# Optimization experiments

Measured on AMD Instinct MI355X. Metric: run time of the kernel, lower is better.

## Reference

```python
import jax, jax.numpy as jnp
import numpy as np


def _rel_agg(h, src, dst, n_nodes):
    """GraphConv(norm='right', weight=False): sum messages at dst, divide by in-degree."""
    msg = jax.ops.segment_sum(h[src], dst, num_segments=n_nodes)          # [N, D]
    deg = jax.ops.segment_sum(jnp.ones(src.shape, h.dtype), dst, num_segments=n_nodes)
    return msg / jnp.maximum(deg, 1.0)[:, None]


def setup_inputs() -> dict:
    key = jax.random.key(0)
    ks = jax.random.split(key, 6)
    N, R, E, D, C = 50000, 4, 400000, 256, 64
    embed = jax.random.normal(ks[0], (N, D), jnp.float32)
    src = jax.random.randint(ks[1], (R, E), 0, N, dtype=jnp.int32)
    dst = jax.random.randint(ks[2], (R, E), 0, N, dtype=jnp.int32)
    b0 = jnp.zeros((D,), jnp.float32)
    w1 = jax.random.normal(ks[3], (R, D, D), jnp.float32) * (1.0 / np.sqrt(D))
    b1 = jnp.zeros((D,), jnp.float32)
    w_out = jax.random.normal(ks[4], (R, D, C), jnp.float32) * (1.0 / np.sqrt(D))
    b_out = jnp.zeros((C,), jnp.float32)
    return {"embed": embed, "src": src, "dst": dst, "b0": b0,
            "w1": w1, "b1": b1, "w_out": w_out, "b_out": b_out}


def reference(embed, src, dst, b0, w1, b1, w_out, b_out):
    N = embed.shape[0]
    R = src.shape[0]
    # Layer 0: weight=False -> sum of per-relation right-normalized aggregations, bias, relu
    h = jnp.zeros_like(embed)
    for r in range(R):
        h = h + _rel_agg(embed, src[r], dst[r], N)
    h = jax.nn.relu(h + b0)
    # Hidden layer: aggregate then per-relation dense weight, summed over relations
    h2 = jnp.zeros((N, w1.shape[2]), embed.dtype)
    for r in range(R):
        h2 = h2 + _rel_agg(h, src[r], dst[r], N) @ w1[r]
    h2 = jax.nn.relu(h2 + b1)
    # Output layer: same, no activation
    out = jnp.zeros((N, w_out.shape[2]), embed.dtype)
    for r in range(R):
        out = out + _rel_agg(h2, src[r], dst[r], N) @ w_out[r]
    return out + b_out
```

## Files before the change

### kernel.cpp

```cpp
#include <hip/hip_runtime.h>


typedef unsigned short ushort_t;
using f32x4  = __attribute__((ext_vector_type(4))) float;
using short8 = __attribute__((ext_vector_type(8))) short;

__device__ inline float bf2f(unsigned s) { return __uint_as_float(s << 16); }
__device__ inline unsigned short f2bf(float f) {
  unsigned u = __float_as_uint(f);
  u += 0x7FFF + ((u >> 16) & 1);
  return (unsigned short)(u >> 16);
}
__device__ inline void u4tof8(const uint4 v, float f[8]) {
  f[0] = bf2f(v.x & 0xffffu); f[1] = bf2f(v.x >> 16);
  f[2] = bf2f(v.y & 0xffffu); f[3] = bf2f(v.y >> 16);
  f[4] = bf2f(v.z & 0xffffu); f[5] = bf2f(v.z >> 16);
  f[6] = bf2f(v.w & 0xffffu); f[7] = bf2f(v.w >> 16);
}

__global__ void rank_k(const int* __restrict__ dst, int E, int Nn,
                       int* __restrict__ cnt, int* __restrict__ rank) {
  int base = (blockIdx.x * blockDim.x + threadIdx.x) * 8;
  int r = blockIdx.y;
  if (base >= E) return;
  const int* dr = dst + (size_t)r * E;
  int* cr = cnt + (size_t)r * Nn;
  int* rk = rank + (size_t)r * E;
  if (base + 7 < E) {
    const int4 a = *reinterpret_cast<const int4*>(dr + base);
    const int4 b = *reinterpret_cast<const int4*>(dr + base + 4);
    int4 ra, rb;
    ra.x = atomicAdd(&cr[a.x], 1); ra.y = atomicAdd(&cr[a.y], 1);
    ra.z = atomicAdd(&cr[a.z], 1); ra.w = atomicAdd(&cr[a.w], 1);
    rb.x = atomicAdd(&cr[b.x], 1); rb.y = atomicAdd(&cr[b.y], 1);
    rb.z = atomicAdd(&cr[b.z], 1); rb.w = atomicAdd(&cr[b.w], 1);
    *reinterpret_cast<int4*>(rk + base) = ra;
    *reinterpret_cast<int4*>(rk + base + 4) = rb;
  } else {
    for (int j = 0; j < 8 && base + j < E; j++)
      rk[base + j] = atomicAdd(&cr[dr[base + j]], 1);
  }
}

__global__ __launch_bounds__(1024) void scanA_k(const int* __restrict__ degcnt, int M,
                                                int* __restrict__ rowptr,
                                                int* __restrict__ blocksum) {
  __shared__ int sm[1024];
  int t = threadIdx.x;
  int g = blockIdx.x * 1024 + t;
  int v = (g < M) ? degcnt[g] : 0;
  sm[t] = v;
  __syncthreads();
  for (int off = 1; off < 1024; off <<= 1) {
    int u = (t >= off) ? sm[t - off] : 0;
    __syncthreads();
    sm[t] += u;
    __syncthreads();
  }
  if (g < M) rowptr[g] = sm[t] - v;
  if (t == 1023) blocksum[blockIdx.x] = sm[1023];
}

__global__ __launch_bounds__(1024) void scanB_k(int* __restrict__ blocksum, int nb) {
  __shared__ int sm[1024];
  int t = threadIdx.x;
  int v = (t < nb) ? blocksum[t] : 0;
  sm[t] = v;
  __syncthreads();
  for (int off = 1; off < 1024; off <<= 1) {
    int u = (t >= off) ? sm[t - off] : 0;
    __syncthreads();
    sm[t] += u;
    __syncthreads();
  }
  if (t < nb) blocksum[t] = sm[t] - v;
}

__global__ __launch_bounds__(1024) void scanC_k(const int* __restrict__ degcnt, int M,
                                                const int* __restrict__ blocksum,
                                                int* __restrict__ rowptr,
                                                float* __restrict__ invdeg) {
  int g = blockIdx.x * 1024 + threadIdx.x;
  if (g < M) {
    int val = rowptr[g] + blocksum[blockIdx.x];
    int dd = degcnt[g];
    rowptr[g] = val;
    invdeg[g] = 1.0f / (float)(dd > 0 ? dd : 1);
    if (g == M - 1) rowptr[M] = val + dd;
  }
}

__global__ void fill_k(const int* __restrict__ src, const int* __restrict__ dst,
                       const int* __restrict__ rank,
                       const int* __restrict__ rowptr, int E, int Nn,
                       int* __restrict__ eidx) {
  int base = (blockIdx.x * blockDim.x + threadIdx.x) * 8;
  int r = blockIdx.y;
  if (base >= E) return;
  const int* dr = dst + (size_t)r * E;
  const int* sr = src + (size_t)r * E;
  const int* rk = rank + (size_t)r * E;
  const int* rp = rowptr + (size_t)r * Nn;
  if (base + 7 < E) {
    const int4 d0 = *reinterpret_cast<const int4*>(dr + base);
    const int4 d1 = *reinterpret_cast<const int4*>(dr + base + 4);
    const int4 s0 = *reinterpret_cast<const int4*>(sr + base);
    const int4 s1 = *reinterpret_cast<const int4*>(sr + base + 4);
    const int4 k0 = *reinterpret_cast<const int4*>(rk + base);
    const int4 k1 = *reinterpret_cast<const int4*>(rk + base + 4);
    eidx[rp[d0.x] + k0.x] = s0.x;
    eidx[rp[d0.y] + k0.y] = s0.y;
    eidx[rp[d0.z] + k0.z] = s0.z;
    eidx[rp[d0.w] + k0.w] = s0.w;
    eidx[rp[d1.x] + k1.x] = s1.x;
    eidx[rp[d1.y] + k1.y] = s1.y;
    eidx[rp[d1.z] + k1.z] = s1.z;
    eidx[rp[d1.w] + k1.w] = s1.w;
  } else {
    for (int j = 0; j < 8 && base + j < E; j++)
      eidx[rp[dr[base + j]] + rk[base + j]] = sr[base + j];
  }
}

__global__ void f2bf_vec_k(const float* __restrict__ in, ushort_t* __restrict__ out,
                           long n4) {
  long i = (long)blockIdx.x * blockDim.x + threadIdx.x;
  if (i < n4) {
    float4 v = *reinterpret_cast<const float4*>(in + i * 4);
    ushort4 o; o.x = f2bf(v.x); o.y = f2bf(v.y); o.z = f2bf(v.z); o.w = f2bf(v.w);
    *reinterpret_cast<ushort4*>(out + i * 4) = o;
  }
}

__global__ void wtrans_k(const float* __restrict__ w, ushort_t* __restrict__ wt,
                         int K, int Nd, int total) {
  int tid = blockIdx.x * blockDim.x + threadIdx.x;
  if (tid < total) {
    int k = tid % K;
    int j = tid / K;
    int c = j % Nd;
    int r = j / Nd;
    wt[(size_t)j * K + k] = f2bf(w[((size_t)r * K + k) * Nd + c]);
  }
}

__global__ __launch_bounds__(256) void pull_gather256_k(
    const ushort_t* __restrict__ x, int xpitch, int rsub,
    const int* __restrict__ eidx,
    const int* __restrict__ rowptr, const float* __restrict__ invdeg,
    int R, int Nn, ushort_t* __restrict__ out, const float* __restrict__ bias) {
  int wv = (blockIdx.x * blockDim.x + threadIdx.x) >> 6;
  int lane = threadIdx.x & 63;
  int node = (wv << 1) + (lane >> 5);
  if (node >= Nn) return;
  int col8 = (lane & 31) << 3;
  float s[8] = {};
  for (int r = 0; r < R; r++) {
    const int* rp = rowptr + (size_t)r * Nn;
    int sb = rp[node], e = rp[node + 1];
    size_t rb = (size_t)(r * rsub + col8);
    float p[8] = {};
    for (int i = sb; i < e; i += 4) {
      int i1 = i + 1 < e ? i + 1 : i;
      int i2 = i + 2 < e ? i + 2 : i;
      int i3 = i + 3 < e ? i + 3 : i;
      float m1 = i + 1 < e ? 1.f : 0.f;
      float m2 = i + 2 < e ? 1.f : 0.f;
      float m3 = i + 3 < e ? 1.f : 0.f;
      const uint4 v0 = *reinterpret_cast<const uint4*>(x + (size_t)eidx[i]  * xpitch + rb);
      const uint4 v1 = *reinterpret_cast<const uint4*>(x + (size_t)eidx[i1] * xpitch + rb);
      const uint4 v2 = *reinterpret_cast<const uint4*>(x + (size_t)eidx[i2] * xpitch + rb);
      const uint4 v3 = *reinterpret_cast<const uint4*>(x + (size_t)eidx[i3] * xpitch + rb);
      float a0[8], a1[8], a2[8], a3[8];
      u4tof8(v0, a0); u4tof8(v1, a1); u4tof8(v2, a2); u4tof8(v3, a3);
#pragma unroll
      for (int j = 0; j < 8; j++)
        p[j] += (a0[j] + m1 * a1[j]) + (m2 * a2[j] + m3 * a3[j]);
    }
    float w = invdeg[(size_t)r * Nn + node];
#pragma unroll
    for (int j = 0; j < 8; j++) s[j] += p[j] * w;
  }
  const float4 ba = *reinterpret_cast<const float4*>(bias + col8);
  const float4 bb = *reinterpret_cast<const float4*>(bias + col8 + 4);
  s[0] += ba.x; s[1] += ba.y; s[2] += ba.z; s[3] += ba.w;
  s[4] += bb.x; s[5] += bb.y; s[6] += bb.z; s[7] += bb.w;
  short8 ov;
#pragma unroll
  for (int j = 0; j < 8; j++) ov[j] = (short)f2bf(fmaxf(s[j], 0.f));
  *reinterpret_cast<short8*>(out + ((size_t)node << 8) + col8) = ov;
}

__global__ __launch_bounds__(256) void pull_out64_k(
    const ushort_t* __restrict__ q, int qpitch,
    const int* __restrict__ eidx,
    const int* __restrict__ rowptr, const float* __restrict__ invdeg,
    int R, int Nn, float* __restrict__ out, const float* __restrict__ bias) {
  int node = (blockIdx.x * blockDim.x + threadIdx.x) >> 6;
  if (node >= Nn) return;
  int lane = threadIdx.x & 63;
  int es = lane >> 4;
  int c4 = (lane & 15) << 2;
  float s[4] = {};
  for (int r = 0; r < R; r++) {
    const int* rp = rowptr + (size_t)r * Nn;
    int sb = rp[node], e = rp[node + 1];
    size_t rb = (size_t)((r << 6) + c4);
    float p[4] = {};
    for (int i = sb + es; i < e; i += 4) {
      const uint2 v = *reinterpret_cast<const uint2*>(q + (size_t)eidx[i] * qpitch + rb);
      p[0] += bf2f(v.x & 0xffffu); p[1] += bf2f(v.x >> 16);
      p[2] += bf2f(v.y & 0xffffu); p[3] += bf2f(v.y >> 16);
    }
    float w = invdeg[(size_t)r * Nn + node];
#pragma unroll
    for (int j = 0; j < 4; j++) s[j] += p[j] * w;
  }
#pragma unroll
  for (int j = 0; j < 4; j++) {
    s[j] += __shfl_xor(s[j], 16, 64);
    s[j] += __shfl_xor(s[j], 32, 64);
  }
  if (es == 0) {
    const float4 bv = *reinterpret_cast<const float4*>(bias + c4);
    float4 o;
    o.x = s[0] + bv.x; o.y = s[1] + bv.y; o.z = s[2] + bv.z; o.w = s[3] + bv.w;
    *reinterpret_cast<float4*>(out + ((size_t)node << 6) + c4) = o;
  }
}

template <int FN>
__global__ __launch_bounds__(256) void gemm_mfma_k(
    const ushort_t* __restrict__ A, const ushort_t* __restrict__ Bt,
    ushort_t* __restrict__ Cp, int M, int K, int Nd) {
  __shared__ ushort_t Atile[128][72];
  const int tid = threadIdx.x;
  const int lane = tid & 63;
  const int wid = tid >> 6;
  const int wr = wid >> 1;
  const int wc = wid & 1;
  const int rowBase = blockIdx.y * 128;
  const int colBase = blockIdx.x * (FN * 32);
  const int l15 = lane & 15;
  const int g = lane >> 4;

  f32x4 acc[4][FN] = {};

  const int srow = tid >> 3;
  const int schunk = tid & 7;

  for (int k0 = 0; k0 < K; k0 += 64) {
#pragma unroll
    for (int i = 0; i < 4; i++) {
      int row = srow + i * 32;
      int grow = rowBase + row;
      if (grow >= M) grow = M - 1;
      short8 v = *reinterpret_cast<const short8*>(A + (size_t)grow * K + k0 + schunk * 8);
      *reinterpret_cast<short8*>(&Atile[row][schunk * 8]) = v;
    }
    __syncthreads();
#pragma unroll
    for (int kk = 0; kk < 2; kk++) {
      short8 a[4], b[FN];
#pragma unroll
      for (int m = 0; m < 4; m++)
        a[m] = *reinterpret_cast<const short8*>(&Atile[wr * 64 + m * 16 + l15][kk * 32 + g * 8]);
#pragma unroll
      for (int n = 0; n < FN; n++) {
        int col = colBase + wc * (FN * 16) + n * 16 + l15;
        b[n] = *reinterpret_cast<const short8*>(Bt + (size_t)col * K + k0 + kk * 32 + g * 8);
      }
#pragma unroll
      for (int m = 0; m < 4; m++)
#pragma unroll
        for (int n = 0; n < FN; n++)
          acc[m][n] = __builtin_amdgcn_mfma_f32_16x16x32_bf16(a[m], b[n], acc[m][n], 0, 0, 0);
    }
    __syncthreads();
  }

#pragma unroll
  for (int n = 0; n < FN; n++) {
    int col = colBase + wc * (FN * 16) + n * 16 + l15;
#pragma unroll
    for (int m = 0; m < 4; m++) {
      int row0 = rowBase + wr * 64 + m * 16 + g * 4;
#pragma unroll
      for (int j = 0; j < 4; j++) {
        int row = row0 + j;
        if (row < M) Cp[(size_t)row * Nd + col] = f2bf(acc[m][n][j]);
      }
    }
  }
}

extern "C" void kernel_launch(void* const* d_in, const int* in_sizes, int n_in,
                              void* d_out, int out_size, void* d_ws, size_t ws_size,
                              hipStream_t stream) {
  const float* embed = (const float*)d_in[0];
  const int* src     = (const int*)d_in[1];
  const int* dst     = (const int*)d_in[2];
  const float* b0    = (const float*)d_in[3];
  const float* w1    = (const float*)d_in[4];
  const float* b1    = (const float*)d_in[5];
  const float* w_out = (const float*)d_in[6];
  const float* b_out = (const float*)d_in[7];
  float* out = (float*)d_out;

  const int D = in_sizes[3];
  const int C = in_sizes[7];
  const int N = in_sizes[0] / D;
  const int R = in_sizes[4] / (D * D);
  const int E = in_sizes[1] / R;
  const int M = R * N;
  const int N1 = R * D;
  const int N2 = R * C;

  char* w = (char*)d_ws;
  size_t off = 0;
  auto carve = [&](size_t bytes) -> void* {
    void* p = w + off;
    off += (bytes + 255) & ~(size_t)255;
    return p;
  };
  ushort_t* ebf  = (ushort_t*)carve((size_t)N * D * 2);
  ushort_t* h    = (ushort_t*)carve((size_t)N * D * 2);
  ushort_t* t    = (ushort_t*)carve((size_t)N * N1 * 2);
  ushort_t* w1t  = (ushort_t*)carve((size_t)N1 * D * 2);
  ushort_t* wot  = (ushort_t*)carve((size_t)N2 * D * 2);
  float* invdeg  = (float*)carve((size_t)M * 4);
  int* rowptr    = (int*)carve(((size_t)M + 1) * 4);
  int* degcnt    = (int*)carve((size_t)M * 4);
  int* eidx      = (int*)carve((size_t)R * E * 4);
  int* blocksum  = (int*)carve(1024 * 4);
  ushort_t* h2 = ebf;
  ushort_t* q  = t;
  int* rank = (int*)t;
  (void)n_in; (void)out_size; (void)ws_size;

  hipMemsetAsync(degcnt, 0, (size_t)M * 4, stream);
  dim3 egrid((E + 2047) / 2048, R);
  rank_k<<<egrid, 256, 0, stream>>>(dst, E, N, degcnt, rank);
  int nblkScan = (M + 1023) / 1024;
  scanA_k<<<nblkScan, 1024, 0, stream>>>(degcnt, M, rowptr, blocksum);
  scanB_k<<<1, 1024, 0, stream>>>(blocksum, nblkScan);
  scanC_k<<<nblkScan, 1024, 0, stream>>>(degcnt, M, blocksum, rowptr, invdeg);
  fill_k<<<egrid, 256, 0, stream>>>(src, dst, rank, rowptr, E, N, eidx);

  long n4 = (long)N * D / 4;
  f2bf_vec_k<<<(int)((n4 + 255) / 256), 256, 0, stream>>>(embed, ebf, n4);
  wtrans_k<<<(N1 * D + 255) / 256, 256, 0, stream>>>(w1, w1t, D, D, N1 * D);
  wtrans_k<<<(N2 * D + 255) / 256, 256, 0, stream>>>(w_out, wot, D, C, N2 * D);

  const int pullBlocks2 = ((N + 1) / 2 * 64 + 255) / 256;
  const int pullBlocks1 = (N * 64 + 255) / 256;

  pull_gather256_k<<<pullBlocks2, 256, 0, stream>>>(ebf, D, 0, eidx, rowptr, invdeg,
                                                    R, N, h, b0);

  {
    dim3 grid(N1 / 128, (N + 127) / 128);
    gemm_mfma_k<4><<<grid, 256, 0, stream>>>(h, w1t, t, N, D, N1);
  }
  pull_gather256_k<<<pullBlocks2, 256, 0, stream>>>(t, N1, D, eidx, rowptr, invdeg,
                                                    R, N, h2, b1);

  {
    dim3 grid(N2 / 128, (N + 127) / 128);
    gemm_mfma_k<4><<<grid, 256, 0, stream>>>(h2, wot, q, N, D, N2);
  }
  pull_out64_k<<<pullBlocks1, 256, 0, stream>>>(q, N2, eidx, rowptr, invdeg,
                                                R, N, out, b_out);
}
```

Before: 519.8 us.

## Fuse hidden-layer aggregation and per-relation GEMM into one kernel

The hidden layer now aggregates the 256-wide features first, per relation, into shared memory. It then multiplies them by that relation's weight slice with MFMA and accumulates across relations inside a new kernel. This replaces the separate GEMM that wrote an N x R*D intermediate and the gather that read it back. The aim is to remove that large intermediate round trip and to gather 256-wide rows instead of 1024-wide ones. In exchange the kernel pairs a latency-bound gather phase with a compute phase and separates them with block barriers, and the weight transpose layout changes to match.

After: 571.0 us. 9.8% more time.

```diff
diff --git a/kernel.cpp b/kernel.cpp
--- a/kernel.cpp
+++ b/kernel.cpp
@@ -191,6 +191,97 @@
   *reinterpret_cast<short8*>(out + ((size_t)node << 8) + col8) = ov;
 }
 
+__global__ __launch_bounds__(256) void fused_l1_k(
+    const ushort_t* __restrict__ h,
+    const ushort_t* __restrict__ Bt,
+    const int* __restrict__ eidx,
+    const int* __restrict__ rowptr,
+    const float* __restrict__ invdeg,
+    int R, int Nn,
+    ushort_t* __restrict__ h2,
+    const float* __restrict__ bias) {
+  __shared__ ushort_t hagg[64][264];
+  const int tid = threadIdx.x;
+  const int lane = tid & 63;
+  const int wid = tid >> 6;
+  const int rowBase = blockIdx.x * 64;
+  const int l15 = lane & 15;
+  const int g = lane >> 4;
+  const int col8 = (lane & 31) << 3;
+  const int half = lane >> 5;
+
+  f32x4 acc[4][4] = {};
+
+  for (int r = 0; r < R; r++) {
+    const int* rp = rowptr + (size_t)r * Nn;
+#pragma unroll
+    for (int step = 0; step < 8; step++) {
+      int rowLocal = wid * 16 + step * 2 + half;
+      int node = rowBase + rowLocal;
+      int cn = node < Nn ? node : Nn - 1;
+      int sb = rp[cn], e = rp[cn + 1];
+      float p[8] = {};
+      for (int i = sb; i < e; i += 4) {
+        int i1 = i + 1 < e ? i + 1 : i;
+        int i2 = i + 2 < e ? i + 2 : i;
+        int i3 = i + 3 < e ? i + 3 : i;
+        float m1 = i + 1 < e ? 1.f : 0.f;
+        float m2 = i + 2 < e ? 1.f : 0.f;
+        float m3 = i + 3 < e ? 1.f : 0.f;
+        const uint4 v0 = *reinterpret_cast<const uint4*>(h + ((size_t)eidx[i]  << 8) + col8);
+        const uint4 v1 = *reinterpret_cast<const uint4*>(h + ((size_t)eidx[i1] << 8) + col8);
+        const uint4 v2 = *reinterpret_cast<const uint4*>(h + ((size_t)eidx[i2] << 8) + col8);
+        const uint4 v3 = *reinterpret_cast<const uint4*>(h + ((size_t)eidx[i3] << 8) + col8);
+        float a0[8], a1[8], a2[8], a3[8];
+        u4tof8(v0, a0); u4tof8(v1, a1); u4tof8(v2, a2); u4tof8(v3, a3);
+#pragma unroll
+        for (int j = 0; j < 8; j++)
+          p[j] += (a0[j] + m1 * a1[j]) + (m2 * a2[j] + m3 * a3[j]);
+      }
+      float w = invdeg[(size_t)r * Nn + cn];
+      short8 ov;
+#pragma unroll
+      for (int j = 0; j < 8; j++) ov[j] = (short)f2bf(p[j] * w);
+      *reinterpret_cast<short8*>(&hagg[rowLocal][col8]) = ov;
+    }
+    __syncthreads();
+#pragma unroll
+    for (int ks = 0; ks < 8; ks++) {
+      short8 a[4], b[4];
+#pragma unroll
+      for (int m = 0; m < 4; m++)
+        a[m] = *reinterpret_cast<const short8*>(&hagg[m * 16 + l15][ks * 32 + g * 8]);
+#pragma unroll
+      for (int n = 0; n < 4; n++) {
+        int col = wid * 64 + n * 16 + l15;
+        b[n] = *reinterpret_cast<const short8*>(Bt + ((size_t)col << 10) + (r << 8) + ks * 32 + g * 8);
+      }
+#pragma unroll
+      for (int m = 0; m < 4; m++)
+#pragma unroll
+        for (int n = 0; n < 4; n++)
+          acc[m][n] = __builtin_amdgcn_mfma_f32_16x16x32_bf16(a[m], b[n], acc[m][n], 0, 0, 0);
+    }
+    __syncthreads();
+  }
+
+#pragma unroll
+  for (int n = 0; n < 4; n++) {
+    int col = wid * 64 + n * 16 + l15;
+    float bv = bias[col];
+#pragma unroll
+    for (int m = 0; m < 4; m++) {
+      int row0 = rowBase + m * 16 + g * 4;
+#pragma unroll
+      for (int j = 0; j < 4; j++) {
+        int row = row0 + j;
+        if (row < Nn)
+          h2[((size_t)row << 8) + col] = f2bf(fmaxf(acc[m][n][j] + bv, 0.f));
+      }
+    }
+  }
+}
+
 __global__ __launch_bounds__(256) void pull_out64_k(
     const ushort_t* __restrict__ q, int qpitch,
     const int* __restrict__ eidx,
@@ -268,7 +359,7 @@
 #pragma unroll
       for (int n = 0; n < FN; n++) {
         int col = colBase + wc * (FN * 16) + n * 16 + l15;
-        b[n] = *reinterpret_cast<const short8*>(Bt + (size_t)col * K + k0 + kk * 32 + g * 8);
+        b[n] = *reinterpret_cast<const short8*>(Bt + (size_t)col * K + kk * 32 + k0 + g * 8);
       }
 #pragma unroll
       for (int m = 0; m < 4; m++)
@@ -326,7 +417,7 @@
   ushort_t* ebf  = (ushort_t*)carve((size_t)N * D * 2);
   ushort_t* h    = (ushort_t*)carve((size_t)N * D * 2);
   ushort_t* t    = (ushort_t*)carve((size_t)N * N1 * 2);
-  ushort_t* w1t  = (ushort_t*)carve((size_t)N1 * D * 2);
+  ushort_t* w1t  = (ushort_t*)carve((size_t)D * N1 * 2);
   ushort_t* wot  = (ushort_t*)carve((size_t)N2 * D * 2);
   float* invdeg  = (float*)carve((size_t)M * 4);
   int* rowptr    = (int*)carve(((size_t)M + 1) * 4);
@@ -349,7 +440,7 @@
 
   long n4 = (long)N * D / 4;
   f2bf_vec_k<<<(int)((n4 + 255) / 256), 256, 0, stream>>>(embed, ebf, n4);
-  wtrans_k<<<(N1 * D + 255) / 256, 256, 0, stream>>>(w1, w1t, D, D, N1 * D);
+  wtrans_k<<<(N1 * D + 255) / 256, 256, 0, stream>>>(w1, w1t, N1, D, N1 * D);
   wtrans_k<<<(N2 * D + 255) / 256, 256, 0, stream>>>(w_out, wot, D, C, N2 * D);
 
   const int pullBlocks2 = ((N + 1) / 2 * 64 + 255) / 256;
@@ -358,12 +449,8 @@
   pull_gather256_k<<<pullBlocks2, 256, 0, stream>>>(ebf, D, 0, eidx, rowptr, invdeg,
                                                     R, N, h, b0);
 
-  {
-    dim3 grid(N1 / 128, (N + 127) / 128);
-    gemm_mfma_k<4><<<grid, 256, 0, stream>>>(h, w1t, t, N, D, N1);
-  }
-  pull_gather256_k<<<pullBlocks2, 256, 0, stream>>>(t, N1, D, eidx, rowptr, invdeg,
-                                                    R, N, h2, b1);
+  fused_l1_k<<<(N + 63) / 64, 256, 0, stream>>>(h, w1t, eidx, rowptr, invdeg,
+                                                R, N, h2, b1);
 
   {
     dim3 grid(N2 / 128, (N + 127) / 128);
```

## Build CSR with destination-sliced counting and cursor-based atomic fill

Applied to the files above, without the earlier changes.

Replaces the rank-recording counting pass with a count-only pass, and the rank-based fill with a fill that claims slots through per-node cursor atomics. Both passes split the grid into 8 destination-range slices so each block's atomics hit a narrower node range, which should improve L2 locality on the counter and cursor arrays. The rank buffer and its write and read traffic go away. In exchange, each edge's dst and src are read 8 times, and neighbour order inside each row is no longer deterministic. That may change floating-point summation order in the gather.

Measured after the change: 588.6 us. 1.13x slower.

```diff
diff --git a/kernel.cpp b/kernel.cpp
--- a/kernel.cpp
+++ b/kernel.cpp
@@ -18,27 +18,33 @@
   f[6] = bf2f(v.w & 0xffffu); f[7] = bf2f(v.w >> 16);
 }
 
-__global__ void rank_k(const int* __restrict__ dst, int E, int Nn,
-                       int* __restrict__ cnt, int* __restrict__ rank) {
-  int base = (blockIdx.x * blockDim.x + threadIdx.x) * 8;
+#define EPT 16
+
+__global__ void count_k(const int* __restrict__ dst, int E, int Nn, int nsl,
+                        int* __restrict__ cnt) {
+  int slice = blockIdx.x & 7;
+  int chunk = blockIdx.x >> 3;
   int r = blockIdx.y;
-  if (base >= E) return;
+  int lo = slice * nsl;
+  int hi = lo + nsl; if (hi > Nn) hi = Nn;
   const int* dr = dst + (size_t)r * E;
   int* cr = cnt + (size_t)r * Nn;
-  int* rk = rank + (size_t)r * E;
-  if (base + 7 < E) {
-    const int4 a = *reinterpret_cast<const int4*>(dr + base);
-    const int4 b = *reinterpret_cast<const int4*>(dr + base + 4);
-    int4 ra, rb;
-    ra.x = atomicAdd(&cr[a.x], 1); ra.y = atomicAdd(&cr[a.y], 1);
-    ra.z = atomicAdd(&cr[a.z], 1); ra.w = atomicAdd(&cr[a.w], 1);
-    rb.x = atomicAdd(&cr[b.x], 1); rb.y = atomicAdd(&cr[b.y], 1);
-    rb.z = atomicAdd(&cr[b.z], 1); rb.w = atomicAdd(&cr[b.w], 1);
-    *reinterpret_cast<int4*>(rk + base) = ra;
-    *reinterpret_cast<int4*>(rk + base + 4) = rb;
-  } else {
-    for (int j = 0; j < 8 && base + j < E; j++)
-      rk[base + j] = atomicAdd(&cr[dr[base + j]], 1);
+  int base = chunk * (256 * EPT) + threadIdx.x * EPT;
+#pragma unroll
+  for (int j0 = 0; j0 < EPT; j0 += 4) {
+    int g = base + j0;
+    if (g + 3 < E) {
+      const int4 d = *reinterpret_cast<const int4*>(dr + g);
+      if (d.x >= lo && d.x < hi) atomicAdd(&cr[d.x], 1);
+      if (d.y >= lo && d.y < hi) atomicAdd(&cr[d.y], 1);
+      if (d.z >= lo && d.z < hi) atomicAdd(&cr[d.z], 1);
+      if (d.w >= lo && d.w < hi) atomicAdd(&cr[d.w], 1);
+    } else {
+      for (int j = 0; j < 4 && g + j < E; j++) {
+        int dd = dr[g + j];
+        if (dd >= lo && dd < hi) atomicAdd(&cr[dd], 1);
+      }
+    }
   }
 }
 
@@ -79,46 +85,47 @@
 __global__ __launch_bounds__(1024) void scanC_k(const int* __restrict__ degcnt, int M,
                                                 const int* __restrict__ blocksum,
                                                 int* __restrict__ rowptr,
+                                                int* __restrict__ cursor,
                                                 float* __restrict__ invdeg) {
   int g = blockIdx.x * 1024 + threadIdx.x;
   if (g < M) {
     int val = rowptr[g] + blocksum[blockIdx.x];
     int dd = degcnt[g];
     rowptr[g] = val;
+    cursor[g] = val;
     invdeg[g] = 1.0f / (float)(dd > 0 ? dd : 1);
     if (g == M - 1) rowptr[M] = val + dd;
   }
 }
 
 __global__ void fill_k(const int* __restrict__ src, const int* __restrict__ dst,
-                       const int* __restrict__ rank,
-                       const int* __restrict__ rowptr, int E, int Nn,
-                       int* __restrict__ eidx) {
-  int base = (blockIdx.x * blockDim.x + threadIdx.x) * 8;
+                       int E, int Nn, int nsl,
+                       int* __restrict__ cursor, int* __restrict__ eidx) {
+  int slice = blockIdx.x & 7;
+  int chunk = blockIdx.x >> 3;
   int r = blockIdx.y;
-  if (base >= E) return;
+  int lo = slice * nsl;
+  int hi = lo + nsl; if (hi > Nn) hi = Nn;
   const int* dr = dst + (size_t)r * E;
   const int* sr = src + (size_t)r * E;
-  const int* rk = rank + (size_t)r * E;
-  const int* rp = rowptr + (size_t)r * Nn;
-  if (base + 7 < E) {
-    const int4 d0 = *reinterpret_cast<const int4*>(dr + base);
-    const int4 d1 = *reinterpret_cast<const int4*>(dr + base + 4);
-    const int4 s0 = *reinterpret_cast<const int4*>(sr + base);
-    const int4 s1 = *reinterpret_cast<const int4*>(sr + base + 4);
-    const int4 k0 = *reinterpret_cast<const int4*>(rk + base);
-    const int4 k1 = *reinterpret_cast<const int4*>(rk + base + 4);
-    eidx[rp[d0.x] + k0.x] = s0.x;
-    eidx[rp[d0.y] + k0.y] = s0.y;
-    eidx[rp[d0.z] + k0.z] = s0.z;
-    eidx[rp[d0.w] + k0.w] = s0.w;
-    eidx[rp[d1.x] + k1.x] = s1.x;
-    eidx[rp[d1.y] + k1.y] = s1.y;
-    eidx[rp[d1.z] + k1.z] = s1.z;
-    eidx[rp[d1.w] + k1.w] = s1.w;
-  } else {
-    for (int j = 0; j < 8 && base + j < E; j++)
-      eidx[rp[dr[base + j]] + rk[base + j]] = sr[base + j];
+  int* cur = cursor + (size_t)r * Nn;
+  int base = chunk * (256 * EPT) + threadIdx.x * EPT;
+#pragma unroll
+  for (int j0 = 0; j0 < EPT; j0 += 4) {
+    int g = base + j0;
+    if (g + 3 < E) {
+      const int4 d = *reinterpret_cast<const int4*>(dr + g);
+      const int4 s = *reinterpret_cast<const int4*>(sr + g);
+      if (d.x >= lo && d.x < hi) eidx[atomicAdd(&cur[d.x], 1)] = s.x;
+      if (d.y >= lo && d.y < hi) eidx[atomicAdd(&cur[d.y], 1)] = s.y;
+      if (d.z >= lo && d.z < hi) eidx[atomicAdd(&cur[d.z], 1)] = s.z;
+      if (d.w >= lo && d.w < hi) eidx[atomicAdd(&cur[d.w], 1)] = s.w;
+    } else {
+      for (int j = 0; j < 4 && g + j < E; j++) {
+        int dd = dr[g + j];
+        if (dd >= lo && dd < hi) eidx[atomicAdd(&cur[dd], 1)] = sr[g + j];
+      }
+    }
   }
 }
 
@@ -331,21 +338,23 @@
   float* invdeg  = (float*)carve((size_t)M * 4);
   int* rowptr    = (int*)carve(((size_t)M + 1) * 4);
   int* degcnt    = (int*)carve((size_t)M * 4);
+  int* cursor    = (int*)carve((size_t)M * 4);
   int* eidx      = (int*)carve((size_t)R * E * 4);
   int* blocksum  = (int*)carve(1024 * 4);
   ushort_t* h2 = ebf;
   ushort_t* q  = t;
-  int* rank = (int*)t;
   (void)n_in; (void)out_size; (void)ws_size;
 
   hipMemsetAsync(degcnt, 0, (size_t)M * 4, stream);
-  dim3 egrid((E + 2047) / 2048, R);
-  rank_k<<<egrid, 256, 0, stream>>>(dst, E, N, degcnt, rank);
+  const int nsl = (N + 7) / 8;
+  const int chunks = (E + 256 * EPT - 1) / (256 * EPT);
+  dim3 egrid(chunks * 8, R);
+  count_k<<<egrid, 256, 0, stream>>>(dst, E, N, nsl, degcnt);
   int nblkScan = (M + 1023) / 1024;
   scanA_k<<<nblkScan, 1024, 0, stream>>>(degcnt, M, rowptr, blocksum);
   scanB_k<<<1, 1024, 0, stream>>>(blocksum, nblkScan);
-  scanC_k<<<nblkScan, 1024, 0, stream>>>(degcnt, M, blocksum, rowptr, invdeg);
-  fill_k<<<egrid, 256, 0, stream>>>(src, dst, rank, rowptr, E, N, eidx);
+  scanC_k<<<nblkScan, 1024, 0, stream>>>(degcnt, M, blocksum, rowptr, cursor, invdeg);
+  fill_k<<<egrid, 256, 0, stream>>>(src, dst, E, N, nsl, cursor, eidx);
 
   long n4 = (long)N * D / 4;
   f2bf_vec_k<<<(int)((n4 + 255) / 256), 256, 0, stream>>>(embed, ebf, n4);
```

## Split 256-wide pull gather into column slices with edge-parallel lanes and shuffle reduction

Applied to the files above, without the earlier changes.

Replaces the half-wave-per-node gather with a scheme where each wave handles one node and one 32-column slice. The 16 lane groups each take every 16th edge and are combined with xor shuffles. Blocks are interleaved across 8 column slices so that adjacent blocks touch the same source rows, and the masked 4-way unroll is dropped. This aims to expose more independent loads per node and better L2 locality per slice. The cost is 8x more waves, each doing short 64-byte loads, repeated reads of rowptr, eidx and invdeg per slice, and a shuffle-reduction overhead. With average degree ~8 per relation, many of the 16 lane groups sit idle.

Result: slower. 959.4 us (+84.6%).

```diff
diff --git a/kernel.cpp b/kernel.cpp
--- a/kernel.cpp
+++ b/kernel.cpp
@@ -144,51 +144,49 @@
   }
 }
 
-__global__ __launch_bounds__(256) void pull_gather256_k(
+__global__ __launch_bounds__(256) void pull_slice256_k(
     const ushort_t* __restrict__ x, int xpitch, int rsub,
     const int* __restrict__ eidx,
     const int* __restrict__ rowptr, const float* __restrict__ invdeg,
     int R, int Nn, ushort_t* __restrict__ out, const float* __restrict__ bias) {
-  int wv = (blockIdx.x * blockDim.x + threadIdx.x) >> 6;
+  int slice = blockIdx.x & 7;
+  int node = ((blockIdx.x >> 3) << 2) + (threadIdx.x >> 6);
+  if (node >= Nn) return;
   int lane = threadIdx.x & 63;
-  int node = (wv << 1) + (lane >> 5);
-  if (node >= Nn) return;
-  int col8 = (lane & 31) << 3;
+  int slot = lane >> 2;
+  int cl = lane & 3;
+  int colOff = slice * 32 + cl * 8;
   float s[8] = {};
   for (int r = 0; r < R; r++) {
     const int* rp = rowptr + (size_t)r * Nn;
     int sb = rp[node], e = rp[node + 1];
-    size_t rb = (size_t)(r * rsub + col8);
+    size_t rb = (size_t)(r * rsub + colOff);
     float p[8] = {};
-    for (int i = sb; i < e; i += 4) {
-      int i1 = i + 1 < e ? i + 1 : i;
-      int i2 = i + 2 < e ? i + 2 : i;
-      int i3 = i + 3 < e ? i + 3 : i;
-      float m1 = i + 1 < e ? 1.f : 0.f;
-      float m2 = i + 2 < e ? 1.f : 0.f;
-      float m3 = i + 3 < e ? 1.f : 0.f;
-      const uint4 v0 = *reinterpret_cast<const uint4*>(x + (size_t)eidx[i]  * xpitch + rb);
-      const uint4 v1 = *reinterpret_cast<const uint4*>(x + (size_t)eidx[i1] * xpitch + rb);
-      const uint4 v2 = *reinterpret_cast<const uint4*>(x + (size_t)eidx[i2] * xpitch + rb);
-      const uint4 v3 = *reinterpret_cast<const uint4*>(x + (size_t)eidx[i3] * xpitch + rb);
-      float a0[8], a1[8], a2[8], a3[8];
-      u4tof8(v0, a0); u4tof8(v1, a1); u4tof8(v2, a2); u4tof8(v3, a3);
-#pragma unroll
-      for (int j = 0; j < 8; j++)
-        p[j] += (a0[j] + m1 * a1[j]) + (m2 * a2[j] + m3 * a3[j]);
+    for (int i = sb + slot; i < e; i += 16) {
+      const uint4 v = *reinterpret_cast<const uint4*>(x + (size_t)eidx[i] * xpitch + rb);
+      float a[8];
+      u4tof8(v, a);
+#pragma unroll
+      for (int j = 0; j < 8; j++) p[j] += a[j];
     }
     float w = invdeg[(size_t)r * Nn + node];
 #pragma unroll
     for (int j = 0; j < 8; j++) s[j] += p[j] * w;
   }
-  const float4 ba = *reinterpret_cast<const float4*>(bias + col8);
-  const float4 bb = *reinterpret_cast<const float4*>(bias + col8 + 4);
-  s[0] += ba.x; s[1] += ba.y; s[2] += ba.z; s[3] += ba.w;
-  s[4] += bb.x; s[5] += bb.y; s[6] += bb.z; s[7] += bb.w;
-  short8 ov;
-#pragma unroll
-  for (int j = 0; j < 8; j++) ov[j] = (short)f2bf(fmaxf(s[j], 0.f));
-  *reinterpret_cast<short8*>(out + ((size_t)node << 8) + col8) = ov;
+#pragma unroll
+  for (int m = 4; m <= 32; m <<= 1)
+#pragma unroll
+    for (int j = 0; j < 8; j++) s[j] += __shfl_xor(s[j], m, 64);
+  if (slot == 0) {
+    const float4 ba = *reinterpret_cast<const float4*>(bias + colOff);
+    const float4 bb = *reinterpret_cast<const float4*>(bias + colOff + 4);
+    s[0] += ba.x; s[1] += ba.y; s[2] += ba.z; s[3] += ba.w;
+    s[4] += bb.x; s[5] += bb.y; s[6] += bb.z; s[7] += bb.w;
+    short8 ov;
+#pragma unroll
+    for (int j = 0; j < 8; j++) ov[j] = (short)f2bf(fmaxf(s[j], 0.f));
+    *reinterpret_cast<short8*>(out + ((size_t)node << 8) + colOff) = ov;
+  }
 }
 
 __global__ __launch_bounds__(256) void pull_out64_k(
@@ -352,18 +350,18 @@
   wtrans_k<<<(N1 * D + 255) / 256, 256, 0, stream>>>(w1, w1t, D, D, N1 * D);
   wtrans_k<<<(N2 * D + 255) / 256, 256, 0, stream>>>(w_out, wot, D, C, N2 * D);
 
-  const int pullBlocks2 = ((N + 1) / 2 * 64 + 255) / 256;
+  const int sliceBlocks = ((N + 3) / 4) * 8;
   const int pullBlocks1 = (N * 64 + 255) / 256;
 
-  pull_gather256_k<<<pullBlocks2, 256, 0, stream>>>(ebf, D, 0, eidx, rowptr, invdeg,
-                                                    R, N, h, b0);
+  pull_slice256_k<<<sliceBlocks, 256, 0, stream>>>(ebf, D, 0, eidx, rowptr, invdeg,
+                                                   R, N, h, b0);
 
   {
     dim3 grid(N1 / 128, (N + 127) / 128);
     gemm_mfma_k<4><<<grid, 256, 0, stream>>>(h, w1t, t, N, D, N1);
   }
-  pull_gather256_k<<<pullBlocks2, 256, 0, stream>>>(t, N1, D, eidx, rowptr, invdeg,
-                                                    R, N, h2, b1);
+  pull_slice256_k<<<sliceBlocks, 256, 0, stream>>>(t, N1, D, eidx, rowptr, invdeg,
+                                                   R, N, h2, b1);
 
   {
     dim3 grid(N2 / 128, (N + 127) / 128);
```
